# Kernel tuning notes

Hardware: AMD Instinct MI355X
Metric: run time of the kernel (lower is better)

The kernel has to match this reference:

```python
import jax, jax.numpy as jnp
import numpy as np

B, L, D = 1, 4096, 1024
H = 16
HD = D // H
SCALE = HD ** -0.5


def setup_inputs() -> dict:
    key = jax.random.key(0)
    k1, k2, k3 = jax.random.split(key, 3)
    X = jax.random.normal(k1, (B, L, D), dtype=jnp.float32)
    # torch Linear default init ~ U(-1/sqrt(fan_in), 1/sqrt(fan_in)); scaled normals are fine for a reference
    Wqkv = jax.random.normal(k2, (D, 3 * D), dtype=jnp.float32) * (D ** -0.5)
    bqkv = jnp.zeros((3 * D,), dtype=jnp.float32)
    Wproj = jax.random.normal(k3, (D, D), dtype=jnp.float32) * (D ** -0.5)
    bproj = jnp.zeros((D,), dtype=jnp.float32)
    return {"X": X, "Wqkv": Wqkv, "bqkv": bqkv, "Wproj": Wproj, "bproj": bproj}


def reference(X, Wqkv, bqkv, Wproj, bproj):
    Bn, Ln, Dn = X.shape
    qkv = X @ Wqkv + bqkv                       # [B, L, 3D]
    qkv = qkv.reshape(Bn, Ln, 3, H, HD)
    q, k, v = qkv[:, :, 0], qkv[:, :, 1], qkv[:, :, 2]   # [B, L, H, HD]
    # attention scores [B, H, L, L] (naive, matches original)
    attn = jnp.einsum('bqhd,bkhd->bhqk', q, k) * SCALE
    causal = jnp.tril(jnp.ones((Ln, Ln), dtype=bool))     # True = keep
    attn = jnp.where(causal, attn, -jnp.inf)
    score = jax.nn.softmax(attn, axis=-1)
    out = jnp.einsum('bhqk,bkhd->bqhd', score, v)         # [B, L, H, HD]
    out = out.reshape(Bn, Ln, Dn)
    return out @ Wproj + bproj
```

## Files before the change

kernel.cpp:

```cpp
#include <hip/hip_runtime.h>
#include <hip/hip_bf16.h>
#include <string.h>


typedef unsigned short ushort_t;
typedef __attribute__((ext_vector_type(8))) short short8;
typedef __attribute__((ext_vector_type(4))) float f32x4;

#define MFMA16(a, b, c) __builtin_amdgcn_mfma_f32_16x16x32_bf16(a, b, c, 0, 0, 0)

static constexpr int Lq = 4096;
static constexpr int Dm = 1024;
static constexpr int NH = 16;
static constexpr int HD = 64;
static constexpr int D3 = 3072;
static constexpr float SCALE_LOG2E = 0.125f * 1.44269504088896340736f;

__device__ __forceinline__ ushort_t f2bf(float f) {
    union { float f; unsigned int u; } x{f};
    unsigned int u = x.u;
    u += 0x7fffu + ((u >> 16) & 1u);
    return (ushort_t)(u >> 16);
}

__device__ __forceinline__ unsigned int cvtpk(float a, float b) {
    unsigned int r;
    asm("v_cvt_pk_bf16_f32 %0, %1, %2" : "=v"(r) : "v"(a), "v"(b));
    return r;
}

__device__ __forceinline__ void gl2lds16(const ushort_t* g, ushort_t* l) {
    __builtin_amdgcn_global_load_lds(
        (const __attribute__((address_space(1))) unsigned int*)g,
        (__attribute__((address_space(3))) unsigned int*)l, 16, 0, 0);
}

__global__ void __launch_bounds__(256)
prep(const float* __restrict__ X, const float* __restrict__ Wqkv,
     const float* __restrict__ Wproj, ushort_t* __restrict__ Xb,
     ushort_t* __restrict__ WqkvT, ushort_t* __restrict__ WprojT) {
    __shared__ float tile[32][33];
    const int bid = blockIdx.x, tid = threadIdx.x;
    if (bid < 4096) {
        int i = (bid * 256 + tid) * 4;
        float4 v = *(const float4*)&X[i];
        ushort_t r[4] = { f2bf(v.x), f2bf(v.y), f2bf(v.z), f2bf(v.w) };
        *(uint2*)&Xb[i] = *(uint2*)r;
        return;
    }
    const float* W; ushort_t* Wt; int Nd, nb, kb;
    if (bid < 7168) {
        int b = bid - 4096; W = Wqkv;  Wt = WqkvT;  Nd = 3072;
        nb = (b % 96) * 32; kb = (b / 96) * 32;
    } else {
        int b = bid - 7168; W = Wproj; Wt = WprojT; Nd = 1024;
        nb = (b % 32) * 32; kb = (b / 32) * 32;
    }
    const int tx = tid & 31, ty = tid >> 5;
    for (int j = 0; j < 32; j += 8)
        tile[ty + j][tx] = W[(size_t)(kb + ty + j) * Nd + nb + tx];
    __syncthreads();
    for (int j = 0; j < 32; j += 8)
        Wt[(size_t)(nb + ty + j) * Dm + kb + tx] = f2bf(tile[tx][ty + j]);
}

__global__ void __launch_bounds__(256, 3)
gemm_qkv(const ushort_t* __restrict__ A, const ushort_t* __restrict__ Bt,
         const float* __restrict__ bias, ushort_t* __restrict__ Cq,
         ushort_t* __restrict__ Vt) {
    __shared__ alignas(16) ushort_t Alds[2][128 * 32];
    __shared__ alignas(16) ushort_t Blds[2][128 * 32];
    const int tid  = threadIdx.x;
    const int lane = tid & 63;
    const int w    = tid >> 6;
    const int quad = lane >> 4;
    const int l16  = lane & 15;
    const int lin0 = blockIdx.y * 32 + blockIdx.x;
    const int lin  = (lin0 & 7) * 96 + (lin0 >> 3);
    const int mbase = (lin & 31) * 128;
    const int nbase = (lin >> 5) * 128;
    const int moff  = (w >> 1) * 64;
    const int noff  = (w & 1) * 64;
    const int K = Dm;

    f32x4 acc[4][4] = {};

    for (int kb = 0; kb < K; kb += 64) {
        __syncthreads();
        #pragma unroll
        for (int c = 0; c < 4; c++) {
            const int id    = c * 256 + w * 64 + lane;
            const int plane = id >> 9;
            const int rem   = id & 511;
            const int row   = rem >> 2, col = (rem & 3) * 8;
            ushort_t* dstA = &Alds[plane][(size_t)((c & 1) * 256 + w * 64) * 8];
            ushort_t* dstB = &Blds[plane][(size_t)((c & 1) * 256 + w * 64) * 8];
            gl2lds16(&A[(size_t)(mbase + row) * K + kb + plane * 32 + col], dstA);
            gl2lds16(&Bt[(size_t)(nbase + row) * K + kb + plane * 32 + col], dstB);
        }
        __syncthreads();
        #pragma unroll
        for (int kk = 0; kk < 2; kk++) {
            short8 a[4], b[4];
            #pragma unroll
            for (int m = 0; m < 4; m++)
                a[m] = *(const short8*)&Alds[kk][(moff + m * 16 + l16) * 32 + quad * 8];
            #pragma unroll
            for (int n = 0; n < 4; n++)
                b[n] = *(const short8*)&Blds[kk][(noff + n * 16 + l16) * 32 + quad * 8];
            #pragma unroll
            for (int m = 0; m < 4; m++)
                #pragma unroll
                for (int n = 0; n < 4; n++)
                    acc[m][n] = MFMA16(a[m], b[n], acc[m][n]);
        }
    }

    if (nbase < 2048) {
        const bool qscale = (nbase < 1024);
        #pragma unroll
        for (int m = 0; m < 4; m++)
            #pragma unroll
            for (int n = 0; n < 4; n++)
                #pragma unroll
                for (int r = 0; r < 4; r++) {
                    int row = mbase + moff + m * 16 + quad * 4 + r;
                    int col = nbase + noff + n * 16 + l16;
                    float v = acc[m][n][r] + bias[col];
                    if (qscale) v *= SCALE_LOG2E;
                    Cq[(size_t)row * D3 + col] = f2bf(v);
                }
    } else {
        const int dbase = nbase - 2048 + noff;
        const size_t kb0 = (size_t)mbase + moff;
        #pragma unroll
        for (int n = 0; n < 4; n++) {
            const float bv = bias[nbase + noff + n * 16 + l16];
            ushort_t* vrow = Vt + (size_t)(dbase + n * 16 + l16) * Lq + kb0 + quad * 16;
            #pragma unroll
            for (int rp = 0; rp < 2; rp++) {
                ushort_t pk[8];
                #pragma unroll
                for (int dr = 0; dr < 2; dr++)
                    #pragma unroll
                    for (int m = 0; m < 4; m++)
                        pk[dr * 4 + m] = f2bf(acc[m][n][2 * rp + dr] + bv);
                *(short8*)(vrow + rp * 8) = *(const short8*)pk;
            }
        }
    }
}

__global__ void __launch_bounds__(1024)
attn_fwd(const ushort_t* __restrict__ qkv, const ushort_t* __restrict__ Vt,
         ushort_t* __restrict__ O) {
    union SMem {
        struct { ushort_t K[2][2][64 * 64]; ushort_t V[2][2][64 * 64]; } kv;
        float Ml[3 * 256 * 35];
    };
    __shared__ SMem sm;

    const int tid  = threadIdx.x;
    const int lane = tid & 63;
    const int w    = tid >> 6;
    const int qtr  = w >> 2;
    const int sub  = w & 3;
    const int quad = lane >> 4;
    const int l16  = lane & 15;
    const int bid  = blockIdx.x;
    const int h    = bid & 15;
    const int p    = bid >> 4;
    const float NEG_INF = -__builtin_inff();

    const ushort_t* kbase = qkv + Dm + h * HD;
    const ushort_t* vbase = Vt + (size_t)h * HD * Lq;

    int koff[2][2];
    #pragma unroll
    for (int s = 0; s < 2; s++) {
        const int tok = (l16 & 3) * 16 + (qtr & 1) * 8 + ((l16 >> 2) & 3) * 2 + s;
        const int fk  = ((l16 & 3) << 1) | ((l16 >> 2) & 1);
        #pragma unroll
        for (int kh = 0; kh < 2; kh++)
            koff[s][kh] = tok * 64 + (((kh * 4 + quad) ^ fk) * 8);
    }
    int voff[4];
    #pragma unroll
    for (int t4 = 0; t4 < 4; t4++) {
        const int row = t4 * 16 + l16;
        voff[t4] = row * 64 + (((((qtr & 1) * 4) + quad) ^ (row & 7)) * 8);
    }
    const int kmc2 = (qtr >> 1) * 64 + (qtr & 1) * 8 + quad * 2;

    const int  tv  = tid & 511;
    const int  rr  = tv >> 3;
    const int  ccK = (tv & 7) ^ ((((rr >> 4) & 3) << 1) | ((rr >> 1) & 1));
    const int  ccV = (tv & 7) ^ (rr & 7);
    const bool isK = (tid < 512);
    const int  dsto = (w & 7) * 512;
    const ushort_t* kse = kbase + (size_t)rr * D3 + ccK * 8;
    const ushort_t* vse = vbase + (size_t)rr * Lq + ccV * 8;

    for (int sel = 0; sel < 2; sel++) {
        const int c      = sel ? (31 - p) : p;
        const int qc     = c * 128;
        const int rounds = c + 1;
        const int qrow0  = qc + sub * 32;

        short8 qf[2][2];
        #pragma unroll
        for (int m = 0; m < 2; m++) {
            const ushort_t* qr = qkv + (size_t)(qrow0 + m * 16 + l16) * D3 + h * HD;
            qf[m][0] = *(const short8*)(qr + quad * 8);
            qf[m][1] = *(const short8*)(qr + 32 + quad * 8);
        }

        f32x4 o[2][4] = {};
        float sacc[2] = { 0.f, 0.f };

        const ushort_t* kp = kse;
        const ushort_t* vp = vse;

        auto stage = [&](int b) {
            if (isK) {
                gl2lds16(kp,           &sm.kv.K[0][b][dsto]);
                gl2lds16(kp + 64 * D3, &sm.kv.K[1][b][dsto]);
            } else {
                gl2lds16(vp,           &sm.kv.V[0][b][dsto]);
                gl2lds16(vp + 64,      &sm.kv.V[1][b][dsto]);
            }
            kp += (size_t)128 * D3;
            vp += 128;
        };

        stage(0);

        for (int r = 0; r < rounds; r++) {
            const int buf = r & 1;
            __syncthreads();
            if (r + 1 < rounds) stage(buf ^ 1);

            const ushort_t* Kb = &sm.kv.K[qtr >> 1][buf][0];
            const ushort_t* Vb = &sm.kv.V[qtr >> 1][buf][0];
            const bool domask = (r == rounds - 1);
            const int qg0 = qrow0 + l16;

            short8 kf[2][2];
            #pragma unroll
            for (int s = 0; s < 2; s++)
                #pragma unroll
                for (int kh = 0; kh < 2; kh++)
                    kf[s][kh] = *(const short8*)&Kb[koff[s][kh]];

            f32x4 st0[2], st1[2];
            #pragma unroll
            for (int s = 0; s < 2; s++) {
                f32x4 t = {};
                t = MFMA16(kf[s][0], qf[0][0], t);
                t = MFMA16(kf[s][1], qf[0][1], t);
                st0[s] = t;
            }

            short8 vf[4];
            #pragma unroll
            for (int t4 = 0; t4 < 4; t4++)
                vf[t4] = *(const short8*)&Vb[voff[t4]];

            #pragma unroll
            for (int s = 0; s < 2; s++) {
                f32x4 t = {};
                t = MFMA16(kf[s][0], qf[1][0], t);
                t = MFMA16(kf[s][1], qf[1][1], t);
                st1[s] = t;
            }

            short8 pP0;
            {
                union { unsigned int u4[4]; short8 s8; } pb;
                #pragma unroll
                for (int s = 0; s < 2; s++) {
                    float e[4];
                    #pragma unroll
                    for (int r4 = 0; r4 < 4; r4++) {
                        float v = st0[s][r4];
                        if (domask && (r * 128 + kmc2 + s + r4 * 16 > qg0))
                            v = NEG_INF;
                        e[r4] = __builtin_amdgcn_exp2f(v);
                    }
                    sacc[0] += (e[0] + e[1]) + (e[2] + e[3]);
                    pb.u4[s * 2]     = cvtpk(e[0], e[1]);
                    pb.u4[s * 2 + 1] = cvtpk(e[2], e[3]);
                }
                pP0 = pb.s8;
            }

            #pragma unroll
            for (int t4 = 0; t4 < 4; t4++)
                o[0][t4] = MFMA16(vf[t4], pP0, o[0][t4]);

            short8 pP1;
            {
                union { unsigned int u4[4]; short8 s8; } pb;
                #pragma unroll
                for (int s = 0; s < 2; s++) {
                    float e[4];
                    #pragma unroll
                    for (int r4 = 0; r4 < 4; r4++) {
                        float v = st1[s][r4];
                        if (domask && (r * 128 + kmc2 + s + r4 * 16 > qg0 + 16))
                            v = NEG_INF;
                        e[r4] = __builtin_amdgcn_exp2f(v);
                    }
                    sacc[1] += (e[0] + e[1]) + (e[2] + e[3]);
                    pb.u4[s * 2]     = cvtpk(e[0], e[1]);
                    pb.u4[s * 2 + 1] = cvtpk(e[2], e[3]);
                }
                pP1 = pb.s8;
            }

            #pragma unroll
            for (int t4 = 0; t4 < 4; t4++)
                o[1][t4] = MFMA16(vf[t4], pP1, o[1][t4]);
        }

        #pragma unroll
        for (int m = 0; m < 2; m++) {
            sacc[m] += __shfl_xor(sacc[m], 16);
            sacc[m] += __shfl_xor(sacc[m], 32);
        }

        __syncthreads();
        if (qtr != 0) {
            float* dst = sm.Ml + (size_t)((qtr - 1) * 256 + sub * 64 + lane) * 35;
            #pragma unroll
            for (int m = 0; m < 2; m++)
                #pragma unroll
                for (int t4 = 0; t4 < 4; t4++)
                    *(f32x4*)(dst + (m * 4 + t4) * 4) = o[m][t4];
            dst[32] = sacc[0];
            dst[33] = sacc[1];
        }
        __syncthreads();
        if (qtr == 0) {
            #pragma unroll
            for (int j = 0; j < 3; j++) {
                const float* src = sm.Ml + (size_t)(j * 256 + sub * 64 + lane) * 35;
                #pragma unroll
                for (int m = 0; m < 2; m++)
                    #pragma unroll
                    for (int t4 = 0; t4 < 4; t4++)
                        o[m][t4] += *(const f32x4*)(src + (m * 4 + t4) * 4);
                sacc[0] += src[32];
                sacc[1] += src[33];
            }
            #pragma unroll
            for (int m = 0; m < 2; m++) {
                const float inv = 1.0f / sacc[m];
                ushort_t* orow = O + (size_t)(qrow0 + m * 16 + l16) * Dm + h * HD;
                #pragma unroll
                for (int t4 = 0; t4 < 4; t4++) {
                    ushort_t pk[4];
                    #pragma unroll
                    for (int r4 = 0; r4 < 4; r4++)
                        pk[r4] = f2bf(o[m][t4][r4] * inv);
                    *(uint2*)(orow + t4 * 16 + quad * 4) = *(const uint2*)pk;
                }
            }
        }
        __syncthreads();
    }
}

__global__ void __launch_bounds__(256, 2)
gemm_proj(const ushort_t* __restrict__ A, const ushort_t* __restrict__ Bt,
          const float* __restrict__ bias, float* __restrict__ C) {
    __shared__ alignas(16) ushort_t Alds[2][128 * 32];
    __shared__ alignas(16) ushort_t Blds[2][64 * 32];
    const int tid  = threadIdx.x;
    const int lane = tid & 63;
    const int w    = tid >> 6;
    const int quad = lane >> 4;
    const int l16  = lane & 15;
    const int lin0 = blockIdx.y * 32 + blockIdx.x;
    const int lin  = (lin0 & 7) * 64 + (lin0 >> 3);
    const int mbase = (lin & 31) * 128;
    const int nbase = (lin >> 5) * 64;
    const int moff  = (w >> 1) * 64;
    const int noff  = (w & 1) * 32;
    const int K = Dm, N = Dm;

    f32x4 acc[4][2] = {};

    for (int kb = 0; kb < K; kb += 64) {
        __syncthreads();
        #pragma unroll
        for (int c = 0; c < 4; c++) {
            const int id    = c * 256 + w * 64 + lane;
            const int plane = id >> 9;
            const int rem   = id & 511;
            const int row   = rem >> 2, col = (rem & 3) * 8;
            gl2lds16(&A[(size_t)(mbase + row) * K + kb + plane * 32 + col],
                     &Alds[plane][(size_t)((c & 1) * 256 + w * 64) * 8]);
        }
        #pragma unroll
        for (int c = 0; c < 2; c++) {
            const int id    = c * 256 + w * 64 + lane;
            const int plane = id >> 8;
            const int rem   = id & 255;
            const int row   = rem >> 2, col = (rem & 3) * 8;
            gl2lds16(&Bt[(size_t)(nbase + row) * K + kb + plane * 32 + col],
                     &Blds[plane][(size_t)(w * 64) * 8]);
        }
        __syncthreads();
        #pragma unroll
        for (int kk = 0; kk < 2; kk++) {
            short8 a[4], b[2];
            #pragma unroll
            for (int m = 0; m < 4; m++)
                a[m] = *(const short8*)&Alds[kk][(moff + m * 16 + l16) * 32 + quad * 8];
            #pragma unroll
            for (int n = 0; n < 2; n++)
                b[n] = *(const short8*)&Blds[kk][(noff + n * 16 + l16) * 32 + quad * 8];
            #pragma unroll
            for (int m = 0; m < 4; m++)
                #pragma unroll
                for (int n = 0; n < 2; n++)
                    acc[m][n] = MFMA16(a[m], b[n], acc[m][n]);
        }
    }

    #pragma unroll
    for (int m = 0; m < 4; m++)
        #pragma unroll
        for (int n = 0; n < 2; n++)
            #pragma unroll
            for (int r = 0; r < 4; r++) {
                int row = mbase + moff + m * 16 + quad * 4 + r;
                int col = nbase + noff + n * 16 + l16;
                C[(size_t)row * N + col] = acc[m][n][r] + bias[col];
            }
}

extern "C" void kernel_launch(void* const* d_in, const int* in_sizes, int n_in,
                              void* d_out, int out_size, void* d_ws, size_t ws_size,
                              hipStream_t stream) {
    const float* X     = (const float*)d_in[0];
    const float* Wqkv  = (const float*)d_in[1];
    const float* bqkv  = (const float*)d_in[2];
    const float* Wproj = (const float*)d_in[3];
    const float* bproj = (const float*)d_in[4];
    float* out = (float*)d_out;

    ushort_t* ws     = (ushort_t*)d_ws;
    ushort_t* Xb     = ws;
    ushort_t* WqkvT  = Xb + (size_t)Lq * Dm;
    ushort_t* WprojT = WqkvT + (size_t)D3 * Dm;
    ushort_t* qkvB   = WprojT + (size_t)Dm * Dm;
    ushort_t* VtB    = qkvB + (size_t)Lq * D3;
    ushort_t* Ob     = VtB + (size_t)NH * HD * Lq;

    prep<<<dim3(8192), 256, 0, stream>>>(X, Wqkv, Wproj, Xb, WqkvT, WprojT);

    gemm_qkv<<<dim3(Lq / 128, D3 / 128), 256, 0, stream>>>(
        Xb, WqkvT, bqkv, qkvB, VtB);

    attn_fwd<<<dim3(256), 1024, 0, stream>>>(qkvB, VtB, Ob);

    gemm_proj<<<dim3(Lq / 128, Dm / 64), 256, 0, stream>>>(
        Ob, WprojT, bproj, out);
}
```

Baseline: 191.6 us.

## Double-buffer LDS tiles in QKV and projection GEMMs to overlap loads with MFMA

Both GEMM main loops are restructured from a single-buffered 64-wide K step, which used two syncs per step, into a two-stage ping-pong over 32-wide K slices. The next slice is prefetched into the alternate LDS buffer while MFMAs run on the current one, with one barrier per step. This is meant to hide global-to-LDS latency behind compute. In exchange there are twice as many loop iterations and barriers per K. Correctness also depends on the async LDS loads being complete before each barrier.

After: 195.4 us. About the same (+2.0%).

```diff
diff --git a/kernel.cpp b/kernel.cpp
--- a/kernel.cpp
+++ b/kernel.cpp
@@ -85,35 +85,36 @@
 
     f32x4 acc[4][4] = {};
 
-    for (int kb = 0; kb < K; kb += 64) {
+    auto stage = [&](int b, int kb) {
+        #pragma unroll
+        for (int c = 0; c < 2; c++) {
+            const int id  = w * 128 + c * 64 + lane;
+            const int row = id >> 2, col = (id & 3) * 8;
+            gl2lds16(&A[(size_t)(mbase + row) * K + kb + col],
+                     &Alds[b][(size_t)(w * 128 + c * 64) * 8]);
+            gl2lds16(&Bt[(size_t)(nbase + row) * K + kb + col],
+                     &Blds[b][(size_t)(w * 128 + c * 64) * 8]);
+        }
+    };
+
+    stage(0, 0);
+    int cur = 0;
+    for (int t = 0; t < 32; t++) {
         __syncthreads();
-        #pragma unroll
-        for (int c = 0; c < 4; c++) {
-            const int id    = c * 256 + w * 64 + lane;
-            const int plane = id >> 9;
-            const int rem   = id & 511;
-            const int row   = rem >> 2, col = (rem & 3) * 8;
-            ushort_t* dstA = &Alds[plane][(size_t)((c & 1) * 256 + w * 64) * 8];
-            ushort_t* dstB = &Blds[plane][(size_t)((c & 1) * 256 + w * 64) * 8];
-            gl2lds16(&A[(size_t)(mbase + row) * K + kb + plane * 32 + col], dstA);
-            gl2lds16(&Bt[(size_t)(nbase + row) * K + kb + plane * 32 + col], dstB);
-        }
-        __syncthreads();
-        #pragma unroll
-        for (int kk = 0; kk < 2; kk++) {
-            short8 a[4], b[4];
-            #pragma unroll
-            for (int m = 0; m < 4; m++)
-                a[m] = *(const short8*)&Alds[kk][(moff + m * 16 + l16) * 32 + quad * 8];
+        if (t + 1 < 32) stage(cur ^ 1, (t + 1) * 32);
+        short8 a[4], b[4];
+        #pragma unroll
+        for (int m = 0; m < 4; m++)
+            a[m] = *(const short8*)&Alds[cur][(moff + m * 16 + l16) * 32 + quad * 8];
+        #pragma unroll
+        for (int n = 0; n < 4; n++)
+            b[n] = *(const short8*)&Blds[cur][(noff + n * 16 + l16) * 32 + quad * 8];
+        #pragma unroll
+        for (int m = 0; m < 4; m++)
             #pragma unroll
             for (int n = 0; n < 4; n++)
-                b[n] = *(const short8*)&Blds[kk][(noff + n * 16 + l16) * 32 + quad * 8];
-            #pragma unroll
-            for (int m = 0; m < 4; m++)
-                #pragma unroll
-                for (int n = 0; n < 4; n++)
-                    acc[m][n] = MFMA16(a[m], b[n], acc[m][n]);
-        }
+                acc[m][n] = MFMA16(a[m], b[n], acc[m][n]);
+        cur ^= 1;
     }
 
     if (nbase < 2048) {
@@ -391,42 +392,40 @@
 
     f32x4 acc[4][2] = {};
 
-    for (int kb = 0; kb < K; kb += 64) {
+    auto stage = [&](int bf, int kb) {
+        #pragma unroll
+        for (int c = 0; c < 2; c++) {
+            const int id  = w * 128 + c * 64 + lane;
+            const int row = id >> 2, col = (id & 3) * 8;
+            gl2lds16(&A[(size_t)(mbase + row) * K + kb + col],
+                     &Alds[bf][(size_t)(w * 128 + c * 64) * 8]);
+        }
+        {
+            const int id  = w * 64 + lane;
+            const int row = id >> 2, col = (id & 3) * 8;
+            gl2lds16(&Bt[(size_t)(nbase + row) * K + kb + col],
+                     &Blds[bf][(size_t)(w * 64) * 8]);
+        }
+    };
+
+    stage(0, 0);
+    int cur = 0;
+    for (int t = 0; t < 32; t++) {
         __syncthreads();
-        #pragma unroll
-        for (int c = 0; c < 4; c++) {
-            const int id    = c * 256 + w * 64 + lane;
-            const int plane = id >> 9;
-            const int rem   = id & 511;
-            const int row   = rem >> 2, col = (rem & 3) * 8;
-            gl2lds16(&A[(size_t)(mbase + row) * K + kb + plane * 32 + col],
-                     &Alds[plane][(size_t)((c & 1) * 256 + w * 64) * 8]);
-        }
-        #pragma unroll
-        for (int c = 0; c < 2; c++) {
-            const int id    = c * 256 + w * 64 + lane;
-            const int plane = id >> 8;
-            const int rem   = id & 255;
-            const int row   = rem >> 2, col = (rem & 3) * 8;
-            gl2lds16(&Bt[(size_t)(nbase + row) * K + kb + plane * 32 + col],
-                     &Blds[plane][(size_t)(w * 64) * 8]);
-        }
-        __syncthreads();
-        #pragma unroll
-        for (int kk = 0; kk < 2; kk++) {
-            short8 a[4], b[2];
-            #pragma unroll
-            for (int m = 0; m < 4; m++)
-                a[m] = *(const short8*)&Alds[kk][(moff + m * 16 + l16) * 32 + quad * 8];
+        if (t + 1 < 32) stage(cur ^ 1, (t + 1) * 32);
+        short8 a[4], b[2];
+        #pragma unroll
+        for (int m = 0; m < 4; m++)
+            a[m] = *(const short8*)&Alds[cur][(moff + m * 16 + l16) * 32 + quad * 8];
+        #pragma unroll
+        for (int n = 0; n < 2; n++)
+            b[n] = *(const short8*)&Blds[cur][(noff + n * 16 + l16) * 32 + quad * 8];
+        #pragma unroll
+        for (int m = 0; m < 4; m++)
             #pragma unroll
             for (int n = 0; n < 2; n++)
-                b[n] = *(const short8*)&Blds[kk][(noff + n * 16 + l16) * 32 + quad * 8];
-            #pragma unroll
-            for (int m = 0; m < 4; m++)
-                #pragma unroll
-                for (int n = 0; n < 2; n++)
-                    acc[m][n] = MFMA16(a[m], b[n], acc[m][n]);
-        }
+                acc[m][n] = MFMA16(a[m], b[n], acc[m][n]);
+        cur ^= 1;
     }
 
     #pragma unroll
```
